# Kernel tuning notes

Measured on AMD Instinct MI355X. Metric: run time of the kernel, lower is better.

The kernel has to match this reference:

```python
import jax, jax.numpy as jnp
import numpy as np

C_IN, CH, HCH, NFFT, HOP, NL, K = 100, 512, 1536, 1024, 256, 8, 4
B, T = 16, 1024

def conv1d(x, w, b=None, pad=0, groups=1):
    # x: [B, Cin, L], w: [Cout, Cin/groups, K]
    y = jax.lax.conv_general_dilated(x, w, (1,), [(pad, pad)],
        dimension_numbers=('NCH', 'OIH', 'NCH'), feature_group_count=groups)
    if b is not None:
        y = y + b[None, :, None]
    return y

def layernorm(x, g, b, eps=1e-5):
    # normalize over last axis (channel), torch LayerNorm semantics (biased var)
    mu = jnp.mean(x, -1, keepdims=True)
    var = jnp.var(x, -1, keepdims=True)
    return (x - mu) * jax.lax.rsqrt(var + eps) * g + b

def setup_inputs() -> dict:
    key = jax.random.key(0)
    ks = jax.random.split(key, 8)
    r = lambda k, s: jax.random.normal(k, s, jnp.float32) * 0.02
    return {
        'x': jax.random.normal(ks[0], (B, C_IN, T), jnp.float32),
        'in_w': r(ks[1], (CH, C_IN, 7)), 'in_b': jnp.zeros((CH,), jnp.float32),
        'norm_g': jnp.ones((CH,), jnp.float32), 'norm_b': jnp.zeros((CH,), jnp.float32),
        'dw_w': r(ks[2], (NL, CH, 1, 7)), 'dw_b': jnp.zeros((NL, CH), jnp.float32),
        'ln_g': jnp.ones((NL, CH), jnp.float32), 'ln_b': jnp.zeros((NL, CH), jnp.float32),
        'pw1_w': r(ks[3], (NL, HCH, CH)), 'pw1_b': jnp.zeros((NL, HCH), jnp.float32),
        'pw2_w': r(ks[4], (NL, CH, HCH)), 'pw2_b': jnp.zeros((NL, CH), jnp.float32),
        'ls': jnp.full((NL, CH), 1.0 / NL, jnp.float32),
        'normL_g': jnp.ones((CH,), jnp.float32), 'normL_b': jnp.zeros((CH,), jnp.float32),
        'out_w': r(ks[5], (NFFT, CH, 1)), 'out_b': jnp.zeros((NFFT,), jnp.float32),
        'ov_w': r(ks[6], (HOP, NFFT, K)),
    }

def reference(x, in_w, in_b, norm_g, norm_b, dw_w, dw_b, ln_g, ln_b,
              pw1_w, pw1_b, pw2_w, pw2_b, ls, normL_g, normL_b, out_w, out_b, ov_w):
    x = conv1d(x, in_w, in_b, pad=3)                                   # [B, CH, T]
    x = layernorm(x.transpose(0, 2, 1), norm_g, norm_b).transpose(0, 2, 1)

    def layer(h, p):
        dw, db, g, b, w1, b1, w2, b2, s = p
        y = conv1d(h, dw, db, pad=3, groups=CH)                        # depthwise 7-tap
        y = layernorm(y.transpose(0, 2, 1), g, b)                      # [B, T, CH]
        y = jnp.einsum('btc,hc->bth', y, w1) + b1                      # pointwise expand
        y = jax.nn.gelu(y, approximate=False)
        y = jnp.einsum('bth,ch->btc', y, w2) + b2                      # pointwise project
        return h + (y * s).transpose(0, 2, 1), None

    x, _ = jax.lax.scan(layer, x, (dw_w, dw_b, ln_g, ln_b, pw1_w, pw1_b, pw2_w, pw2_b, ls))
    x = layernorm(x.transpose(0, 2, 1), normL_g, normL_b).transpose(0, 2, 1)
    o = conv1d(x, out_w, out_b, pad=0)                                 # [B, NFFT, T]
    # --- overlap_add ---
    o = conv1d(o, ov_w, None, pad=K - 1)                               # [B, HOP, L], L = T + K - 1
    Bn, C, L = o.shape
    pad_size = C * K - L + K - 1
    o = jnp.pad(o, ((0, 0), (0, 0), (0, pad_size)))
    idx = (jnp.arange(L)[None, :] + jnp.arange(C)[:, None] * (C * K - 1)) % L  # [C, L]
    o = jnp.take_along_axis(o, jnp.broadcast_to(idx[None], (Bn, C, L)), axis=2)
    o = jnp.sum(o, axis=1, keepdims=True)                              # [B, 1, L]
    return o[..., K // 2 : L - K // 2 + 1]                             # [B, 1, T]
```

## Files before the change

kernel.cpp:

```cpp
#include <hip/hip_runtime.h>

#define B_    16
#define CIN   100
#define T_    1024
#define CH_   512
#define HCH_  1536
#define NL_   8
#define NFFT_ 1024
#define HOP_  256
#define BT    (B_ * T_)
#define L_    1027
#define OROWS 1032
#define KIN   704

typedef __bf16 bf16x8 __attribute__((ext_vector_type(8)));
typedef float f32x4 __attribute__((ext_vector_type(4)));
typedef short s16x8 __attribute__((ext_vector_type(8)));

__device__ __forceinline__ short f2b(float f) {
  unsigned u = __float_as_uint(f);
  u += 0x7fffu + ((u >> 16) & 1u);
  return (short)(u >> 16);
}
__device__ __forceinline__ float b2f(short s) {
  return __uint_as_float(((unsigned)(unsigned short)s) << 16);
}

__device__ __forceinline__ float fast_gelu(float x) {
  float ax = fabsf(x);
  float z = 0.7978845608f * ax * (1.f + 0.044715f * ax * ax);
  float e = __expf(-2.f * z);
  float th = 1.f - 2.f * e * __builtin_amdgcn_rcpf(1.f + e);
  float g = copysignf(th, x);
  return 0.5f * x * (1.f + g);
}

__device__ __forceinline__ void gl2lds16(const void* g, void* l) {
  __builtin_amdgcn_global_load_lds(
      (__attribute__((address_space(1))) void*)g,
      (__attribute__((address_space(3))) void*)l, 16, 0, 0);
}

__global__ __launch_bounds__(256) void k_cvt(const float* __restrict__ s,
                                             short* __restrict__ d, int n) {
  for (int i = blockIdx.x * 256 + threadIdx.x; i < n; i += gridDim.x * 256)
    d[i] = f2b(s[i]);
}

__global__ __launch_bounds__(256) void k_cvt_ov(const float* __restrict__ w,
                                                short* __restrict__ d) {
  const int n = 4 * HOP_ * NFFT_;
  for (int i = blockIdx.x * 256 + threadIdx.x; i < n; i += gridDim.x * 256) {
    int k = i >> 18;
    int rem = i & 0x3FFFF;
    int c = rem >> 10, nn = rem & 1023;
    d[i] = f2b(w[((size_t)c * NFFT_ + nn) * 4 + k]);
  }
}

__global__ __launch_bounds__(256) void k_cvt_inw(const float* __restrict__ w,
                                                 short* __restrict__ d) {
  const int n = CH_ * KIN;
  for (int i = blockIdx.x * 256 + threadIdx.x; i < n; i += gridDim.x * 256) {
    int c = i / KIN, e = i - c * KIN;
    d[i] = (e < 700) ? f2b(w[c * 700 + e]) : (short)0;
  }
}

__global__ __launch_bounds__(256) void k_cvt_dwt(const float* __restrict__ w,
                                                 float* __restrict__ d) {
  const int n = NL_ * 7 * CH_;
  for (int i = blockIdx.x * 256 + threadIdx.x; i < n; i += gridDim.x * 256) {
    int l = i / (7 * CH_), r = i - l * 7 * CH_;
    int k = r >> 9, c = r & 511;
    d[i] = w[((size_t)l * CH_ + c) * 7 + k];
  }
}

__global__ __launch_bounds__(256) void k_im2col(const float* __restrict__ x,
                                                short* __restrict__ xim) {
  const int total = BT * KIN;
  for (int i = blockIdx.x * 256 + threadIdx.x; i < total; i += gridDim.x * 256) {
    int m = i / KIN, e = i - m * KIN;
    int b = m >> 10, t = m & 1023;
    int ci = e / 7, k = e - ci * 7;
    int tt = t + k - 3;
    float v = (e < 700 && tt >= 0 && tt < T_) ? x[((b * CIN + ci) << 10) + tt] : 0.f;
    xim[i] = f2b(v);
  }
}

__global__ __launch_bounds__(256) void k_zeropad(short* __restrict__ o1p) {
  int i = blockIdx.x * 256 + threadIdx.x;
  int b = i >> 13;
  int r8 = (i >> 10) & 7;
  int nn = i & 1023;
  int row = r8 < 4 ? r8 : (OROWS - 8 + r8);
  o1p[((size_t)b * OROWS + row) * NFFT_ + nn] = 0;
}

__global__ __launch_bounds__(256) void k_lnb(const short* __restrict__ in,
                                             short* __restrict__ outp,
                                             const float* __restrict__ g,
                                             const float* __restrict__ bta) {
  int row = blockIdx.x, tid = threadIdx.x;
  unsigned u = *reinterpret_cast<const unsigned*>(&in[(size_t)row * CH_ + tid * 2]);
  float v0 = __uint_as_float(u << 16);
  float v1 = __uint_as_float(u & 0xffff0000u);
  float s = v0 + v1, q = v0 * v0 + v1 * v1;
#pragma unroll
  for (int o = 32; o > 0; o >>= 1) { s += __shfl_down(s, o); q += __shfl_down(q, o); }
  __shared__ float sh[8];
  int wid = tid >> 6, lane = tid & 63;
  if (lane == 0) { sh[wid] = s; sh[wid + 4] = q; }
  __syncthreads();
  float S = sh[0] + sh[1] + sh[2] + sh[3];
  float Q = sh[4] + sh[5] + sh[6] + sh[7];
  float mu  = S * (1.f / 512.f);
  float var = Q * (1.f / 512.f) - mu * mu;
  float r = rsqrtf(var + 1e-5f);
  float x0 = (v0 - mu) * r * g[tid * 2]     + bta[tid * 2];
  float x1 = (v1 - mu) * r * g[tid * 2 + 1] + bta[tid * 2 + 1];
  unsigned o = ((unsigned)(unsigned short)f2b(x0)) |
               (((unsigned)(unsigned short)f2b(x1)) << 16);
  *reinterpret_cast<unsigned*>(&outp[(size_t)row * CH_ + tid * 2]) = o;
}

__global__ __launch_bounds__(256) void k_dwln(const short* __restrict__ h,
                                              const float* __restrict__ dwt,
                                              const float* __restrict__ dwb,
                                              const float* __restrict__ g,
                                              const float* __restrict__ bta,
                                              short* __restrict__ yb) {
  int b = blockIdx.x, t0 = blockIdx.y * 32;
  int tid = threadIdx.x, lane = tid & 63, w = tid >> 6;
  __shared__ short hs[38][512];
  for (int e = tid; e < 38 * 64; e += 256) {
    int row = e >> 6, seg = (e & 63) << 3;
    int t = t0 - 3 + row;
    s16x8 v = {};
    if (t >= 0 && t < T_)
      v = *reinterpret_cast<const s16x8*>(&h[((size_t)((b << 10) + t)) * CH_ + seg]);
    *reinterpret_cast<s16x8*>(&hs[row][seg]) = v;
  }
  const int c0 = lane << 3;
  float wk[7][8];
#pragma unroll
  for (int k = 0; k < 7; ++k) {
    f32x4 lo = *reinterpret_cast<const f32x4*>(&dwt[k * CH_ + c0]);
    f32x4 hi = *reinterpret_cast<const f32x4*>(&dwt[k * CH_ + c0 + 4]);
#pragma unroll
    for (int j = 0; j < 4; ++j) { wk[k][j] = lo[j]; wk[k][j + 4] = hi[j]; }
  }
  float bb[8], gg[8], be[8];
  {
    f32x4 a = *reinterpret_cast<const f32x4*>(&dwb[c0]);
    f32x4 b4 = *reinterpret_cast<const f32x4*>(&dwb[c0 + 4]);
    f32x4 c = *reinterpret_cast<const f32x4*>(&g[c0]);
    f32x4 d = *reinterpret_cast<const f32x4*>(&g[c0 + 4]);
    f32x4 e = *reinterpret_cast<const f32x4*>(&bta[c0]);
    f32x4 f = *reinterpret_cast<const f32x4*>(&bta[c0 + 4]);
#pragma unroll
    for (int j = 0; j < 4; ++j) {
      bb[j] = a[j]; bb[j + 4] = b4[j];
      gg[j] = c[j]; gg[j + 4] = d[j];
      be[j] = e[j]; be[j + 4] = f[j];
    }
  }
  __syncthreads();
#pragma unroll
  for (int i = 0; i < 8; ++i) {
    int r = w * 8 + i;
    float acc[8];
#pragma unroll
    for (int j = 0; j < 8; ++j) acc[j] = bb[j];
#pragma unroll
    for (int k = 0; k < 7; ++k) {
      s16x8 hv = *reinterpret_cast<const s16x8*>(&hs[r + k][c0]);
#pragma unroll
      for (int j = 0; j < 8; ++j) acc[j] += b2f(hv[j]) * wk[k][j];
    }
    float s = 0.f, q = 0.f;
#pragma unroll
    for (int j = 0; j < 8; ++j) { s += acc[j]; q += acc[j] * acc[j]; }
#pragma unroll
    for (int o = 32; o > 0; o >>= 1) { s += __shfl_xor(s, o); q += __shfl_xor(q, o); }
    float mu  = s * (1.f / 512.f);
    float var = q * (1.f / 512.f) - mu * mu;
    float rr = rsqrtf(var + 1e-5f);
    s16x8 ov;
#pragma unroll
    for (int j = 0; j < 8; ++j) ov[j] = f2b((acc[j] - mu) * rr * gg[j] + be[j]);
    *reinterpret_cast<s16x8*>(&yb[((size_t)((b << 10) + t0 + r)) * CH_ + c0]) = ov;
  }
}

template <int MODE>
__global__ __launch_bounds__(256) void k_mgemm(const short* __restrict__ A,
                                               const short* __restrict__ Bw,
                                               const float* __restrict__ bias,
                                               const float* __restrict__ scale,
                                               short* __restrict__ obf,
                                               int N, int K) {
  __shared__ __align__(16) short smem[4 * 128 * 64];
  const int tid = threadIdx.x;
  const int lane = tid & 63, w = tid >> 6;
  const int id = blockIdx.x;
  const int ny = N >> 7;
  const int g8 = id >> 3;
  const int gq = g8 / ny;
  const int mt = (id & 7) + (gq << 3);
  const int nt_ = g8 - gq * ny;
  const int m0 = mt << 7, n0 = nt_ << 7;
  const int wr = (w >> 1) * 64, wc = (w & 1) * 64;
  f32x4 acc[4][4];
#pragma unroll
  for (int i = 0; i < 4; ++i)
#pragma unroll
    for (int j = 0; j < 4; ++j) acc[i][j] = (f32x4){0.f, 0.f, 0.f, 0.f};

  const short* Ab = A + (size_t)m0 * K;
  const short* Bb = Bw + (size_t)n0 * K;
  int r_[4], kk_[4];
#pragma unroll
  for (int j = 0; j < 4; ++j) {
    int c = tid + j * 256;
    r_[j] = c >> 3;
    kk_[j] = (((c & 7) ^ (r_[j] & 7)) * 8);
  }
  const int ar = wr + (lane & 15);
  const int br = wc + (lane & 15);
  const int hi = lane >> 4;
  const int nsteps = K >> 6;

  auto stage = [&](int buf, int k0) {
    short* Sa = smem + buf * 16384;
    short* Sb = Sa + 8192;
#pragma unroll
    for (int j = 0; j < 4; ++j)
      gl2lds16(Ab + (size_t)r_[j] * K + k0 + kk_[j], Sa + (j * 256 + w * 64) * 8);
#pragma unroll
    for (int j = 0; j < 4; ++j)
      gl2lds16(Bb + (size_t)r_[j] * K + k0 + kk_[j], Sb + (j * 256 + w * 64) * 8);
  };

  stage(0, 0);
  asm volatile("s_waitcnt vmcnt(0)" ::: "memory");
  __syncthreads();
  for (int t = 0; t < nsteps; ++t) {
    const int cur = t & 1;
    if (t + 1 < nsteps) stage(cur ^ 1, (t + 1) << 6);
    const short* As = smem + cur * 16384;
    const short* Bs = As + 8192;
#pragma unroll
    for (int ks = 0; ks < 2; ++ks) {
      bf16x8 a[4], b[4];
#pragma unroll
      for (int f = 0; f < 4; ++f) {
        int row = ar + f * 16;
        a[f] = *reinterpret_cast<const bf16x8*>(&As[row * 64 + (((ks * 4 + hi) ^ (row & 7)) * 8)]);
      }
#pragma unroll
      for (int f = 0; f < 4; ++f) {
        int row = br + f * 16;
        b[f] = *reinterpret_cast<const bf16x8*>(&Bs[row * 64 + (((ks * 4 + hi) ^ (row & 7)) * 8)]);
      }
#pragma unroll
      for (int fi = 0; fi < 4; ++fi)
#pragma unroll
        for (int fj = 0; fj < 4; ++fj)
          acc[fi][fj] = __builtin_amdgcn_mfma_f32_16x16x32_bf16(a[fi], b[fj], acc[fi][fj], 0, 0, 0);
    }
    asm volatile("s_waitcnt vmcnt(0)" ::: "memory");
    __syncthreads();
  }
  short* Cl = smem;
  const int colbase = wc + (lane & 15);
#pragma unroll
  for (int fj = 0; fj < 4; ++fj) {
    int cl = colbase + fj * 16;
    int n = n0 + cl;
    float bi = bias[n];
    float sc = (MODE == 2) ? scale[n] : 0.f;
#pragma unroll
    for (int fi = 0; fi < 4; ++fi) {
#pragma unroll
      for (int r = 0; r < 4; ++r) {
        int rl = wr + (hi << 2) + fi * 16 + r;
        float v = acc[fi][fj][r] + bi;
        if (MODE == 1) v = fast_gelu(v);
        if (MODE == 2) v *= sc;
        Cl[rl * 128 + (cl ^ (((rl >> 2) & 3) << 4))] = f2b(v);
      }
    }
  }
  __syncthreads();
  const int cs = (lane & 15) * 8;
#pragma unroll
  for (int it = 0; it < 8; ++it) {
    int rl = w * 32 + it * 4 + (lane >> 4);
    s16x8 v = *reinterpret_cast<const s16x8*>(&Cl[rl * 128 + (cs ^ (((rl >> 2) & 3) << 4))]);
    int m = m0 + rl;
    if (MODE == 2) {
      size_t idx = (size_t)m * N + n0 + cs;
      s16x8 hv = *reinterpret_cast<const s16x8*>(&obf[idx]);
      s16x8 o;
#pragma unroll
      for (int j = 0; j < 8; ++j) o[j] = f2b(b2f(hv[j]) + b2f(v[j]));
      *reinterpret_cast<s16x8*>(&obf[idx]) = o;
    } else if (MODE == 3) {
      int bb = m >> 10, t = m & 1023;
      *reinterpret_cast<s16x8*>(&obf[((size_t)(bb * OROWS + 4 + t)) * NFFT_ + n0 + cs]) = v;
    } else {
      *reinterpret_cast<s16x8*>(&obf[(size_t)m * N + n0 + cs]) = v;
    }
  }
}

__global__ __launch_bounds__(256) void k_ovgemm(const short* __restrict__ o1p,
                                                const short* __restrict__ ovb,
                                                float* __restrict__ o2) {
  __shared__ __align__(16) short As[136 * 64];
  __shared__ __align__(16) short Bs[128 * 64];
  const int tid = threadIdx.x;
  const int lane = tid & 63, w = tid >> 6;
  const int l0 = blockIdx.x * 128, c0 = blockIdx.y * 128, b = blockIdx.z;
  const int wr = (w >> 1) * 64, wc = (w & 1) * 64;
  f32x4 acc[4][4];
#pragma unroll
  for (int i = 0; i < 4; ++i)
#pragma unroll
    for (int j = 0; j < 4; ++j) acc[i][j] = (f32x4){0.f, 0.f, 0.f, 0.f};

  const short* Ab = o1p + (size_t)b * OROWS * NFFT_;
  const int ar = wr + (lane & 15);
  const int br = wc + (lane & 15);
  const int hi = lane >> 4;
  const int sl_row = lane >> 3;
  const int sl_j   = lane & 7;

  for (int k0 = 0; k0 < NFFT_; k0 += 64) {
    for (int c = w; c < 17; c += 4) {
      int lr = c * 8 + sl_row;
      int gr = l0 + 1 + lr;
      if (gr > OROWS - 1) gr = OROWS - 1;
      int j = sl_j ^ (lr & 7);
      gl2lds16(Ab + (size_t)gr * NFFT_ + k0 + j * 8, As + c * 512);
    }
#pragma unroll
    for (int ksh = 0; ksh < 4; ++ksh) {
      const short* Bb = ovb + ((size_t)(ksh * HOP_ + c0)) * NFFT_;
#pragma unroll
      for (int c = 0; c < 4; ++c) {
        int ch = w * 4 + c;
        int lr = ch * 8 + sl_row;
        int j = sl_j ^ (lr & 7);
        gl2lds16(Bb + (size_t)lr * NFFT_ + k0 + j * 8, Bs + ch * 512);
      }
      asm volatile("s_waitcnt vmcnt(0)" ::: "memory");
      __syncthreads();
#pragma unroll
      for (int ks = 0; ks < 2; ++ks) {
        bf16x8 a[4], bfr[4];
#pragma unroll
        for (int f = 0; f < 4; ++f) {
          int row = ar + f * 16 + ksh;
          a[f] = *reinterpret_cast<const bf16x8*>(&As[row * 64 + (((ks * 4 + hi) ^ (row & 7)) * 8)]);
        }
#pragma unroll
        for (int f = 0; f < 4; ++f) {
          int row = br + f * 16;
          bfr[f] = *reinterpret_cast<const bf16x8*>(&Bs[row * 64 + (((ks * 4 + hi) ^ (row & 7)) * 8)]);
        }
#pragma unroll
        for (int fi = 0; fi < 4; ++fi)
#pragma unroll
          for (int fj = 0; fj < 4; ++fj)
            acc[fi][fj] = __builtin_amdgcn_mfma_f32_16x16x32_bf16(a[fi], bfr[fj], acc[fi][fj], 0, 0, 0);
      }
      __syncthreads();
    }
  }
  const int lb = l0 + wr + (hi << 2);
  const int cb = c0 + wc + (lane & 15);
#pragma unroll
  for (int fj = 0; fj < 4; ++fj) {
    int c = cb + fj * 16;
#pragma unroll
    for (int fi = 0; fi < 4; ++fi) {
#pragma unroll
      for (int r = 0; r < 4; ++r) {
        int l = lb + fi * 16 + r;
        if (l < L_) o2[((size_t)b * L_ + l) * HOP_ + c] = acc[fi][fj][r];
      }
    }
  }
}

__global__ __launch_bounds__(256) void k_oadd(const float* __restrict__ o2,
                                              float* __restrict__ out) {
  int b = blockIdx.x;
  int t = blockIdx.y * 256 + threadIdx.x;
  int m = t + 2;
  float s = 0.f;
  for (int c = 0; c < HOP_; ++c) {
    s += o2[((size_t)b * L_ + m) * HOP_ + c];
    m -= 4;
    if (m < 0) m += L_;
  }
  out[b * T_ + t] = s;
}

extern "C" void kernel_launch(void* const* d_in, const int* in_sizes, int n_in,
                              void* d_out, int out_size, void* d_ws, size_t ws_size,
                              hipStream_t stream) {
  const float* x      = (const float*)d_in[0];
  const float* in_w   = (const float*)d_in[1];
  const float* in_b   = (const float*)d_in[2];
  const float* norm_g = (const float*)d_in[3];
  const float* norm_b = (const float*)d_in[4];
  const float* dw_w   = (const float*)d_in[5];
  const float* dw_b   = (const float*)d_in[6];
  const float* ln_g   = (const float*)d_in[7];
  const float* ln_b   = (const float*)d_in[8];
  const float* pw1_w  = (const float*)d_in[9];
  const float* pw1_b  = (const float*)d_in[10];
  const float* pw2_w  = (const float*)d_in[11];
  const float* pw2_b  = (const float*)d_in[12];
  const float* ls     = (const float*)d_in[13];
  const float* normLg = (const float*)d_in[14];
  const float* normLb = (const float*)d_in[15];
  const float* out_w  = (const float*)d_in[16];
  const float* out_b  = (const float*)d_in[17];
  const float* ov_w   = (const float*)d_in[18];
  float* out = (float*)d_out;

  char* p = (char*)d_ws;
  short* hb   = (short*)p; p += (size_t)BT * CH_ * 2;
  short* yb   = (short*)p; p += (size_t)BT * CH_ * 2;
  short* zb   = (short*)p; p += (size_t)BT * HCH_ * 2;
  short* pw1b = (short*)p; p += (size_t)NL_ * HCH_ * CH_ * 2;
  short* pw2b = (short*)p; p += (size_t)NL_ * CH_ * HCH_ * 2;
  short* owb  = (short*)p; p += (size_t)NFFT_ * CH_ * 2;
  short* ovb  = (short*)p; p += (size_t)4 * HOP_ * NFFT_ * 2;
  float* dwt  = (float*)p; p += (size_t)NL_ * 7 * CH_ * 4;
  short* xim  = zb;
  short* wib  = zb + (size_t)BT * KIN;
  short* hbL  = yb;
  short* o1p  = zb;
  float* o2   = (float*)hb;

  k_cvt<<<4096, 256, 0, stream>>>(pw1_w, pw1b, NL_ * HCH_ * CH_);
  k_cvt<<<4096, 256, 0, stream>>>(pw2_w, pw2b, NL_ * CH_ * HCH_);
  k_cvt<<<2048, 256, 0, stream>>>(out_w, owb, NFFT_ * CH_);
  k_cvt_ov<<<4096, 256, 0, stream>>>(ov_w, ovb);
  k_cvt_inw<<<1408, 256, 0, stream>>>(in_w, wib);
  k_cvt_dwt<<<112, 256, 0, stream>>>(dw_w, dwt);
  k_im2col<<<8192, 256, 0, stream>>>(x, xim);

  k_mgemm<0><<<512, 256, 0, stream>>>(xim, wib, in_b, nullptr, hb, CH_, KIN);
  k_lnb<<<BT, 256, 0, stream>>>(hb, hb, norm_g, norm_b);
  for (int l = 0; l < NL_; ++l) {
    k_dwln<<<dim3(B_, T_ / 32), 256, 0, stream>>>(
        hb, dwt + (size_t)l * 7 * CH_, dw_b + l * CH_,
        ln_g + l * CH_, ln_b + l * CH_, yb);
    k_mgemm<1><<<1536, 256, 0, stream>>>(
        yb, pw1b + (size_t)l * HCH_ * CH_, pw1_b + l * HCH_, nullptr, zb,
        HCH_, CH_);
    k_mgemm<2><<<512, 256, 0, stream>>>(
        zb, pw2b + (size_t)l * CH_ * HCH_, pw2_b + l * CH_, ls + l * CH_, hb,
        CH_, HCH_);
  }
  k_lnb<<<BT, 256, 0, stream>>>(hb, hbL, normLg, normLb);
  k_mgemm<3><<<1024, 256, 0, stream>>>(hbL, owb, out_b, nullptr, o1p, NFFT_, CH_);
  k_zeropad<<<512, 256, 0, stream>>>(o1p);
  k_ovgemm<<<dim3(9, 2, 16), 256, 0, stream>>>(o1p, ovb, o2);
  k_oadd<<<dim3(B_, 4), 256, 0, stream>>>(o2, out);
}
```

Baseline: 889.8 us.

## Double-buffer overlap GEMM, halve its column tile, and vectorize weight conversion

Restructures the overlap-add GEMM so it double-buffers the A and B tiles in LDS. The next k-slice and shift are prefetched while MFMAs run on the current buffers. The column tile shrinks from 128 to 64 and the grid doubles, which raises block count from 288 to 576 to better fill the CUs. The fp32-to-bf16 weight conversion kernels also move to float4 loads, and the ov-weight transpose reads each 4-tap group once. The cost is more LDS per block and less reuse of A per block.

```diff
diff --git a/kernel.cpp b/kernel.cpp
--- a/kernel.cpp
+++ b/kernel.cpp
@@ -16,6 +16,7 @@
 typedef __bf16 bf16x8 __attribute__((ext_vector_type(8)));
 typedef float f32x4 __attribute__((ext_vector_type(4)));
 typedef short s16x8 __attribute__((ext_vector_type(8)));
+typedef short s16x4 __attribute__((ext_vector_type(4)));
 
 __device__ __forceinline__ short f2b(float f) {
   unsigned u = __float_as_uint(f);
@@ -41,20 +42,22 @@
       (__attribute__((address_space(3))) void*)l, 16, 0, 0);
 }
 
-__global__ __launch_bounds__(256) void k_cvt(const float* __restrict__ s,
-                                             short* __restrict__ d, int n) {
-  for (int i = blockIdx.x * 256 + threadIdx.x; i < n; i += gridDim.x * 256)
-    d[i] = f2b(s[i]);
+__global__ __launch_bounds__(256) void k_cvt4(const float* __restrict__ s,
+                                              short* __restrict__ d, int n4) {
+  for (int i = blockIdx.x * 256 + threadIdx.x; i < n4; i += gridDim.x * 256) {
+    f32x4 v = *reinterpret_cast<const f32x4*>(&s[i * 4]);
+    s16x4 o = {f2b(v[0]), f2b(v[1]), f2b(v[2]), f2b(v[3])};
+    *reinterpret_cast<s16x4*>(&d[i * 4]) = o;
+  }
 }
 
 __global__ __launch_bounds__(256) void k_cvt_ov(const float* __restrict__ w,
                                                 short* __restrict__ d) {
-  const int n = 4 * HOP_ * NFFT_;
+  const int n = HOP_ * NFFT_;
   for (int i = blockIdx.x * 256 + threadIdx.x; i < n; i += gridDim.x * 256) {
-    int k = i >> 18;
-    int rem = i & 0x3FFFF;
-    int c = rem >> 10, nn = rem & 1023;
-    d[i] = f2b(w[((size_t)c * NFFT_ + nn) * 4 + k]);
+    f32x4 v = *reinterpret_cast<const f32x4*>(&w[(size_t)i * 4]);
+#pragma unroll
+    for (int k = 0; k < 4; ++k) d[(size_t)k * n + i] = f2b(v[k]);
   }
 }
 
@@ -320,17 +323,17 @@
 __global__ __launch_bounds__(256) void k_ovgemm(const short* __restrict__ o1p,
                                                 const short* __restrict__ ovb,
                                                 float* __restrict__ o2) {
-  __shared__ __align__(16) short As[136 * 64];
-  __shared__ __align__(16) short Bs[128 * 64];
+  __shared__ __align__(16) short As2[2][136 * 64];
+  __shared__ __align__(16) short Bs2[2][64 * 64];
   const int tid = threadIdx.x;
   const int lane = tid & 63, w = tid >> 6;
-  const int l0 = blockIdx.x * 128, c0 = blockIdx.y * 128, b = blockIdx.z;
-  const int wr = (w >> 1) * 64, wc = (w & 1) * 64;
-  f32x4 acc[4][4];
+  const int l0 = blockIdx.x * 128, c0 = blockIdx.y * 64, b = blockIdx.z;
+  const int wr = (w >> 1) * 64, wc = (w & 1) * 32;
+  f32x4 acc[4][2];
 #pragma unroll
   for (int i = 0; i < 4; ++i)
 #pragma unroll
-    for (int j = 0; j < 4; ++j) acc[i][j] = (f32x4){0.f, 0.f, 0.f, 0.f};
+    for (int j = 0; j < 2; ++j) acc[i][j] = (f32x4){0.f, 0.f, 0.f, 0.f};
 
   const short* Ab = o1p + (size_t)b * OROWS * NFFT_;
   const int ar = wr + (lane & 15);
@@ -338,53 +341,74 @@
   const int hi = lane >> 4;
   const int sl_row = lane >> 3;
   const int sl_j   = lane & 7;
-
-  for (int k0 = 0; k0 < NFFT_; k0 += 64) {
-    for (int c = w; c < 17; c += 4) {
-      int lr = c * 8 + sl_row;
+  int br_[2], bk_[2];
+#pragma unroll
+  for (int j = 0; j < 2; ++j) {
+    int c = tid + j * 256;
+    br_[j] = c >> 3;
+    bk_[j] = ((c & 7) ^ (br_[j] & 7)) * 8;
+  }
+
+  auto stageA = [&](int buf, int k0) {
+    for (int cg = w; cg < 17; cg += 4) {
+      int lr = cg * 8 + sl_row;
       int gr = l0 + 1 + lr;
       if (gr > OROWS - 1) gr = OROWS - 1;
       int j = sl_j ^ (lr & 7);
-      gl2lds16(Ab + (size_t)gr * NFFT_ + k0 + j * 8, As + c * 512);
-    }
-#pragma unroll
-    for (int ksh = 0; ksh < 4; ++ksh) {
-      const short* Bb = ovb + ((size_t)(ksh * HOP_ + c0)) * NFFT_;
-#pragma unroll
-      for (int c = 0; c < 4; ++c) {
-        int ch = w * 4 + c;
-        int lr = ch * 8 + sl_row;
-        int j = sl_j ^ (lr & 7);
-        gl2lds16(Bb + (size_t)lr * NFFT_ + k0 + j * 8, Bs + ch * 512);
+      gl2lds16(Ab + (size_t)gr * NFFT_ + k0 + j * 8, &As2[buf][cg * 512]);
+    }
+  };
+  auto stageB = [&](int buf, int k0, int ksh) {
+    const short* Bb = ovb + ((size_t)(ksh * HOP_ + c0)) * NFFT_;
+#pragma unroll
+    for (int j = 0; j < 2; ++j)
+      gl2lds16(Bb + (size_t)br_[j] * NFFT_ + k0 + bk_[j],
+               &Bs2[buf][(j * 256 + w * 64) * 8]);
+  };
+
+  int ab = 0, bb = 0;
+  stageA(0, 0);
+  stageB(0, 0, 0);
+  asm volatile("s_waitcnt vmcnt(0)" ::: "memory");
+  __syncthreads();
+  for (int t = 0; t < 64; ++t) {
+    const int ksh = t & 3;
+    const int nt = t + 1;
+    if (nt < 64) {
+      int nk0 = (nt >> 2) << 6;
+      if ((nt & 3) == 0) stageA(ab ^ 1, nk0);
+      stageB(bb ^ 1, nk0, nt & 3);
+    }
+    const short* As = As2[ab];
+    const short* Bs = Bs2[bb];
+#pragma unroll
+    for (int ks = 0; ks < 2; ++ks) {
+      bf16x8 a[4], bfr[2];
+#pragma unroll
+      for (int f = 0; f < 4; ++f) {
+        int row = ar + f * 16 + ksh;
+        a[f] = *reinterpret_cast<const bf16x8*>(&As[row * 64 + (((ks * 4 + hi) ^ (row & 7)) * 8)]);
       }
-      asm volatile("s_waitcnt vmcnt(0)" ::: "memory");
-      __syncthreads();
-#pragma unroll
-      for (int ks = 0; ks < 2; ++ks) {
-        bf16x8 a[4], bfr[4];
-#pragma unroll
-        for (int f = 0; f < 4; ++f) {
-          int row = ar + f * 16 + ksh;
-          a[f] = *reinterpret_cast<const bf16x8*>(&As[row * 64 + (((ks * 4 + hi) ^ (row & 7)) * 8)]);
-        }
-#pragma unroll
-        for (int f = 0; f < 4; ++f) {
-          int row = br + f * 16;
-          bfr[f] = *reinterpret_cast<const bf16x8*>(&Bs[row * 64 + (((ks * 4 + hi) ^ (row & 7)) * 8)]);
-        }
-#pragma unroll
-        for (int fi = 0; fi < 4; ++fi)
-#pragma unroll
-          for (int fj = 0; fj < 4; ++fj)
-            acc[fi][fj] = __builtin_amdgcn_mfma_f32_16x16x32_bf16(a[fi], bfr[fj], acc[fi][fj], 0, 0, 0);
+#pragma unroll
+      for (int f = 0; f < 2; ++f) {
+        int row = br + f * 16;
+        bfr[f] = *reinterpret_cast<const bf16x8*>(&Bs[row * 64 + (((ks * 4 + hi) ^ (row & 7)) * 8)]);
       }
-      __syncthreads();
-    }
+#pragma unroll
+      for (int fi = 0; fi < 4; ++fi)
+#pragma unroll
+        for (int fj = 0; fj < 2; ++fj)
+          acc[fi][fj] = __builtin_amdgcn_mfma_f32_16x16x32_bf16(a[fi], bfr[fj], acc[fi][fj], 0, 0, 0);
+    }
+    asm volatile("s_waitcnt vmcnt(0)" ::: "memory");
+    __syncthreads();
+    bb ^= 1;
+    if (ksh == 3) ab ^= 1;
   }
   const int lb = l0 + wr + (hi << 2);
   const int cb = c0 + wc + (lane & 15);
 #pragma unroll
-  for (int fj = 0; fj < 4; ++fj) {
+  for (int fj = 0; fj < 2; ++fj) {
     int c = cb + fj * 16;
 #pragma unroll
     for (int fi = 0; fi < 4; ++fi) {
@@ -450,10 +474,10 @@
   short* o1p  = zb;
   float* o2   = (float*)hb;
 
-  k_cvt<<<4096, 256, 0, stream>>>(pw1_w, pw1b, NL_ * HCH_ * CH_);
-  k_cvt<<<4096, 256, 0, stream>>>(pw2_w, pw2b, NL_ * CH_ * HCH_);
-  k_cvt<<<2048, 256, 0, stream>>>(out_w, owb, NFFT_ * CH_);
-  k_cvt_ov<<<4096, 256, 0, stream>>>(ov_w, ovb);
+  k_cvt4<<<4096, 256, 0, stream>>>(pw1_w, pw1b, NL_ * HCH_ * CH_ / 4);
+  k_cvt4<<<4096, 256, 0, stream>>>(pw2_w, pw2b, NL_ * CH_ * HCH_ / 4);
+  k_cvt4<<<512, 256, 0, stream>>>(out_w, owb, NFFT_ * CH_ / 4);
+  k_cvt_ov<<<1024, 256, 0, stream>>>(ov_w, ovb);
   k_cvt_inw<<<1408, 256, 0, stream>>>(in_w, wib);
   k_cvt_dwt<<<112, 256, 0, stream>>>(dw_w, dwt);
   k_im2col<<<8192, 256, 0, stream>>>(x, xim);
@@ -474,6 +498,6 @@
   k_lnb<<<BT, 256, 0, stream>>>(hb, hbL, normLg, normLb);
   k_mgemm<3><<<1024, 256, 0, stream>>>(hbL, owb, out_b, nullptr, o1p, NFFT_, CH_);
   k_zeropad<<<512, 256, 0, stream>>>(o1p);
-  k_ovgemm<<<dim3(9, 2, 16), 256, 0, stream>>>(o1p, ovb, o2);
+  k_ovgemm<<<dim3(9, 4, 16), 256, 0, stream>>>(o1p, ovb, o2);
   k_oadd<<<dim3(B_, 4), 256, 0, stream>>>(o2, out);
 }
```

Measured after the change: 885.7 us. About the same (-0.5%).
